# Kernel optimization log

Hardware: AMD Instinct MI355X
Metric: run time of the kernel (lower is better)

## Reference

```python
import jax, jax.numpy as jnp
import numpy as np

B, S, T, H, NH, NL = 16, 128, 64, 128, 8, 4
DH = H // NH
FF = 2 * H
SCALE = 1.0 / float(np.sqrt(DH))


def _ln(x, s, b):
    m = x.mean(-1, keepdims=True)
    v = ((x - m) ** 2).mean(-1, keepdims=True)
    return (x - m) * jax.lax.rsqrt(v + 1e-5) * s + b


def _block(x, mask, p):
    Wq, bq, Wk, bk, Wv, bv, Wo, bo, s1, c1, W1, d1, W2, d2, s2, c2 = p
    N, L, _ = x.shape
    q = (x @ Wq + bq).reshape(N, L, NH, DH)
    k = (x @ Wk + bk).reshape(N, L, NH, DH)
    v = (x @ Wv + bv).reshape(N, L, NH, DH)
    scores = jnp.einsum('nqhd,nkhd->nhqk', q, k) * SCALE
    scores = jnp.where(mask[:, None, :, :], scores, -1e9)
    a = jax.nn.softmax(scores, axis=-1)
    o = jnp.einsum('nhqk,nkhd->nqhd', a, v).reshape(N, L, H)
    x = _ln(x + o @ Wo + bo, s1, c1)
    h = jax.nn.relu(x @ W1 + d1)
    return _ln(x + h @ W2 + d2, s2, c2)


def setup_inputs():
    key = jax.random.key(0)
    ks = jax.random.split(key, 16)
    g = lambda k, shape: jax.random.normal(k, shape, jnp.float32) * 0.02
    return {
        'polylines': jax.random.normal(ks[0], (B, S, T, H), jnp.float32),
        'lengths': jax.random.randint(ks[1], (B, S), 0, T + 1),
        'proj_w': g(ks[2], (H, H)), 'proj_b': jnp.zeros((H,), jnp.float32),
        'proj_ln_s': jnp.ones((H,), jnp.float32), 'proj_ln_b': jnp.zeros((H,), jnp.float32),
        'pos_emb': g(ks[3], (1, T, H)),
        'Wq': g(ks[4], (NL, H, H)), 'bq': jnp.zeros((NL, H), jnp.float32),
        'Wk': g(ks[5], (NL, H, H)), 'bk': jnp.zeros((NL, H), jnp.float32),
        'Wv': g(ks[6], (NL, H, H)), 'bv': jnp.zeros((NL, H), jnp.float32),
        'Wo': g(ks[7], (NL, H, H)), 'bo': jnp.zeros((NL, H), jnp.float32),
        'ln1_s': jnp.ones((NL, H), jnp.float32), 'ln1_b': jnp.zeros((NL, H), jnp.float32),
        'W1': g(ks[8], (NL, H, FF)), 'b1': jnp.zeros((NL, FF), jnp.float32),
        'W2': g(ks[9], (NL, FF, H)), 'b2': jnp.zeros((NL, H), jnp.float32),
        'ln2_s': jnp.ones((NL, H), jnp.float32), 'ln2_b': jnp.zeros((NL, H), jnp.float32),
    }


def reference(polylines, lengths, proj_w, proj_b, proj_ln_s, proj_ln_b, pos_emb,
              Wq, bq, Wk, bk, Wv, bv, Wo, bo, ln1_s, ln1_b, W1, b1, W2, b2, ln2_s, ln2_b):
    # valid[b,s,t] = t < lengths[b,s]; lengths==0 -> polyline absent (fully padded)
    valid = jnp.arange(T)[None, None, :] < lengths[:, :, None]  # [B,S,T]
    x = jnp.where(valid[..., None], polylines, -1.0)            # -1 pad as in np.pad(constant_values=-1)
    # mask_temporal[b,s] = outer(valid[b,s], valid[b,s])
    mask_t = (valid[:, :, :, None] & valid[:, :, None, :]).reshape(B * S, T, T)
    # mask_spatial[b,t] = outer(valid[b,:,t], valid[b,:,t])
    vs = jnp.transpose(valid, (0, 2, 1))                        # [B,T,S]
    mask_s = (vs[:, :, :, None] & vs[:, :, None, :]).reshape(B * T, S, S)

    x = x.reshape(B * S, T, H)
    x = jax.nn.relu(_ln(x @ proj_w + proj_b, proj_ln_s, proj_ln_b))  # MLP: Linear->LN->ReLU
    x = x + pos_emb[:, :T, :]

    mask = mask_t
    for i in range(NL):
        if i == NL // 2:
            # switch from temporal to spatial attention: [B*S,T,H] -> [B*T,S,H]
            x = x.reshape(B, S, T, H).transpose(0, 2, 1, 3).reshape(B * T, S, H)
            mask = mask_s
        p = (Wq[i], bq[i], Wk[i], bk[i], Wv[i], bv[i], Wo[i], bo[i],
             ln1_s[i], ln1_b[i], W1[i], b1[i], W2[i], b2[i], ln2_s[i], ln2_b[i])
        x = _block(x, mask, p)
    # faithful to original final reshape (treats [B*T,S,H] buffer as [B,S,T,H])
    return x.reshape(B, S, T, H)[:, 0, :]
```

## Files before the change

kernel.cpp:

```cpp
#include <hip/hip_runtime.h>

typedef short short8 __attribute__((ext_vector_type(8)));
typedef short short4_t __attribute__((ext_vector_type(4)));
typedef float floatx4 __attribute__((ext_vector_type(4)));
typedef unsigned short ushort_t;

#define B_ 16
#define S_ 128
#define T_ 64
#define H_ 128
#define FF_ 256
#define SCALEQK 0.25f

#define EPI_BIAS 0
#define EPI_RELU 1
#define EPI_LNRES 2
#define EPI_PROJ 3

#define OFFP 0
#define OFFQ(l) (16384 + (l) * 65536)
#define OFFK(l) (OFFQ(l) + 16384)
#define OFFV(l) (OFFQ(l) + 32768)
#define OFFO(l) (OFFQ(l) + 49152)
#define OFFW1(l) (278528 + (l) * 65536)
#define OFFW2(l) (OFFW1(l) + 32768)

__device__ __forceinline__ float b2f(ushort_t u) {
    union { unsigned int i; float f; } x; x.i = ((unsigned int)u) << 16; return x.f;
}
__device__ __forceinline__ ushort_t f2b(float f) {
    union { float f; unsigned int i; } x; x.f = f;
    unsigned int r = x.i + 0x7fffu + ((x.i >> 16) & 1u);
    return (ushort_t)(r >> 16);
}
__device__ __forceinline__ int pack2b(float a, float b) {
    return (int)f2b(a) | ((int)f2b(b) << 16);
}

struct WtEnt { const float* src; int N; int K; int nclog2; int dstoff; };
struct WtArgs { WtEnt e[25]; };

__global__ __launch_bounds__(256) void wt_kernel(WtArgs a, ushort_t* __restrict__ dst) {
    WtEnt ent = a.e[blockIdx.x];
    const int tiles_c = ent.N >> 5;
    const int nt = (ent.K >> 5) * tiles_c;
    const int t = blockIdx.y;
    if (t >= nt) return;
    const int tc = t & (tiles_c - 1);
    const int tr = t >> ent.nclog2;
    __shared__ float ld[32 * 33];
    const int tid = threadIdx.x;
#pragma unroll
    for (int i = 0; i < 4; ++i) {
        int e = tid + i * 256;
        int rr = e >> 5, cc = e & 31;
        ld[rr * 33 + cc] = ent.src[(tr * 32 + rr) * ent.N + tc * 32 + cc];
    }
    __syncthreads();
    ushort_t* d = dst + ent.dstoff;
#pragma unroll
    for (int i = 0; i < 4; ++i) {
        int e = tid + i * 256;
        int rr = e >> 5, cc = e & 31;
        d[(tc * 32 + rr) * ent.K + tr * 32 + cc] = f2b(ld[cc * 33 + rr]);
    }
}

template<int K, int EPI, bool PAD, bool FINAL, bool MULTI, bool OUTB, bool AB16>
__global__ __launch_bounds__(256, 2) void gemm_mfma(
    const void* __restrict__ Av, int lda,
    const ushort_t* wt0, const ushort_t* wt1, const ushort_t* wt2,
    const float* b0, const float* b1, const float* b2,
    const float* __restrict__ resid, int rstride,
    const float* __restrict__ lns, const float* __restrict__ lnb,
    const float* __restrict__ pos, const int* __restrict__ lens,
    void* o0, void* o1, void* o2,
    int Ntot)
{
    __shared__ ushort_t aL[128 * 136];
    __shared__ ushort_t wL[128 * 136];

    const int tid = threadIdx.x;
    const int lane = tid & 63, wv = tid >> 6;
    const size_t rowbase = (size_t)blockIdx.x * 128;

    const ushort_t* wT; const float* bias; void* out; int cbase;
    if (MULTI) {
        int sel = blockIdx.y;
        wT = sel == 0 ? wt0 : (sel == 1 ? wt1 : wt2);
        bias = sel == 0 ? b0 : (sel == 1 ? b1 : b2);
        out = sel == 0 ? o0 : (sel == 1 ? o1 : o2);
        cbase = 0;
    } else {
        wT = wt0; bias = b0; out = o0; cbase = blockIdx.y * 128;
    }

    floatx4 acc[2][8];
#pragma unroll
    for (int a = 0; a < 2; ++a)
#pragma unroll
        for (int c = 0; c < 8; ++c) acc[a][c] = (floatx4){0.f, 0.f, 0.f, 0.f};

    const int arow = wv * 32 + (lane & 15);
    const int koff = (lane >> 4) * 8;

    for (int kc = 0; kc < K; kc += 128) {
        if (kc) __syncthreads();
#pragma unroll
        for (int it = 0; it < 8; ++it) {
            int e8 = tid + it * 256;
            int row = e8 >> 4, kg = e8 & 15;
            int kk = kc + kg * 8;
            short8 val;
            if (AB16) {
                val = *(const short8*)((const ushort_t*)Av + (size_t)(rowbase + row) * lda + kk);
            } else {
                const float* Af = (const float*)Av + (size_t)(rowbase + row) * lda + kk;
                float f[8];
                *(float4*)(f) = *(const float4*)(Af);
                *(float4*)(f + 4) = *(const float4*)(Af + 4);
                if (PAD) {
                    int r = (int)(rowbase + row);
                    if ((r & 63) >= lens[r >> 6]) {
#pragma unroll
                        for (int q = 0; q < 8; ++q) f[q] = -1.0f;
                    }
                }
#pragma unroll
                for (int q = 0; q < 8; ++q) val[q] = (short)f2b(f[q]);
            }
            *(short8*)&aL[row * 136 + kg * 8] = val;
        }
#pragma unroll
        for (int it = 0; it < 8; ++it) {
            int e8 = tid + it * 256;
            int n = e8 >> 4, kg = e8 & 15;
            *(short8*)&wL[n * 136 + kg * 8] =
                *(const short8*)&wT[(size_t)(cbase + n) * K + kc + kg * 8];
        }
        __syncthreads();
#pragma unroll
        for (int k0 = 0; k0 < 128; k0 += 32) {
            short8 a0 = *(const short8*)&aL[arow * 136 + k0 + koff];
            short8 a1 = *(const short8*)&aL[(arow + 16) * 136 + k0 + koff];
#pragma unroll
            for (int ct = 0; ct < 8; ++ct) {
                short8 b = *(const short8*)&wL[(ct * 16 + (lane & 15)) * 136 + k0 + koff];
                acc[0][ct] = __builtin_amdgcn_mfma_f32_16x16x32_bf16(a0, b, acc[0][ct], 0, 0, 0);
                acc[1][ct] = __builtin_amdgcn_mfma_f32_16x16x32_bf16(a1, b, acc[1][ct], 0, 0, 0);
            }
        }
    }

    const int col16 = lane & 15;
    const int rgrp = (lane >> 4) * 4;
    float bcol[8], lnsc[8], lnbc[8];
#pragma unroll
    for (int ct = 0; ct < 8; ++ct) bcol[ct] = bias[cbase + ct * 16 + col16];
    if (EPI == EPI_LNRES || EPI == EPI_PROJ) {
#pragma unroll
        for (int ct = 0; ct < 8; ++ct) {
            lnsc[ct] = lns[ct * 16 + col16];
            lnbc[ct] = lnb[ct * 16 + col16];
        }
    }

#pragma unroll
    for (int rt = 0; rt < 2; ++rt) {
        const int rbase = wv * 32 + rt * 16 + rgrp;
#pragma unroll
        for (int ct = 0; ct < 8; ++ct)
#pragma unroll
            for (int rg = 0; rg < 4; ++rg) {
                float v = acc[rt][ct][rg] + bcol[ct];
                if (EPI == EPI_LNRES)
                    v += resid[(rowbase + rbase + rg) * (size_t)rstride + ct * 16 + col16];
                acc[rt][ct][rg] = v;
            }
        if (EPI == EPI_LNRES || EPI == EPI_PROJ) {
            float mean[4], rstd[4];
#pragma unroll
            for (int rg = 0; rg < 4; ++rg) {
                float s = 0.f;
#pragma unroll
                for (int ct = 0; ct < 8; ++ct) s += acc[rt][ct][rg];
                s += __shfl_xor(s, 1); s += __shfl_xor(s, 2);
                s += __shfl_xor(s, 4); s += __shfl_xor(s, 8);
                mean[rg] = s * (1.f / 128.f);
            }
#pragma unroll
            for (int rg = 0; rg < 4; ++rg) {
                float s = 0.f;
#pragma unroll
                for (int ct = 0; ct < 8; ++ct) {
                    float d = acc[rt][ct][rg] - mean[rg];
                    s += d * d;
                }
                s += __shfl_xor(s, 1); s += __shfl_xor(s, 2);
                s += __shfl_xor(s, 4); s += __shfl_xor(s, 8);
                rstd[rg] = rsqrtf(s * (1.f / 128.f) + 1e-5f);
            }
#pragma unroll
            for (int ct = 0; ct < 8; ++ct)
#pragma unroll
                for (int rg = 0; rg < 4; ++rg)
                    acc[rt][ct][rg] = (acc[rt][ct][rg] - mean[rg]) * rstd[rg] * lnsc[ct] + lnbc[ct];
        }
#pragma unroll
        for (int ct = 0; ct < 8; ++ct)
#pragma unroll
            for (int rg = 0; rg < 4; ++rg) {
                size_t grow = rowbase + rbase + rg;
                int col = cbase + ct * 16 + col16;
                float v = acc[rt][ct][rg];
                if (EPI == EPI_RELU) v = fmaxf(v, 0.f);
                if (EPI == EPI_PROJ)
                    v = fmaxf(v, 0.f) + pos[((int)grow & 63) * H_ + ct * 16 + col16];
                if (FINAL) {
                    int b = (int)(grow >> 7), s = (int)(grow & 127);
                    if (s < T_) ((float*)out)[((size_t)(b * T_ + s)) * H_ + col] = v;
                } else if (OUTB) {
                    ((ushort_t*)out)[grow * (size_t)Ntot + col] = f2b(v);
                } else {
                    ((float*)out)[grow * (size_t)Ntot + col] = v;
                }
            }
    }
}

__global__ __launch_bounds__(256, 1) void attn_s(
    ushort_t* qo, const ushort_t* __restrict__ kk, const ushort_t* __restrict__ vv,
    const int* __restrict__ lens)
{
    __shared__ float kL[128 * 36];
    __shared__ float vL[128 * 36];
    __shared__ int vldL[128];
    const int tid = threadIdx.x;
    const int b = blockIdx.x, hp = blockIdx.y;
    const size_t rowg = (size_t)b * 128;

    if (tid < 128) vldL[tid] = (lens[b * 128 + tid] > 0) ? 1 : 0;
#pragma unroll
    for (int it = 0; it < 2; ++it) {
        int e8 = tid + it * 256;
        int j = e8 >> 2, dg = e8 & 3;
        short8 k8 = *(const short8*)&kk[(rowg + j) * 128 + hp * 32 + dg * 8];
        short8 v8 = *(const short8*)&vv[(rowg + j) * 128 + hp * 32 + dg * 8];
        float* kd = &kL[j * 36 + dg * 8];
        float* vd = &vL[j * 36 + dg * 8];
#pragma unroll
        for (int q = 0; q < 8; ++q) { kd[q] = b2f((ushort_t)k8[q]); vd[q] = b2f((ushort_t)v8[q]); }
    }
    __syncthreads();

    const int hl = tid >> 7;
    const int i = tid & 127;
    const int hc = hl * 16;
    const int h = hp * 2 + hl;

    float qf[16];
    {
        const short8* qp = (const short8*)&qo[(rowg + i) * 128 + h * 16];
        short8 q0 = qp[0], q1 = qp[1];
#pragma unroll
        for (int q = 0; q < 8; ++q) { qf[q] = b2f((ushort_t)q0[q]); qf[8 + q] = b2f((ushort_t)q1[q]); }
    }

    float sc[128];
    const bool iv = vldL[i] != 0;
#pragma unroll
    for (int j = 0; j < 128; ++j) {
        const float* kr = &kL[j * 36 + hc];
        float s = 0.f;
#pragma unroll
        for (int d = 0; d < 16; ++d) s = fmaf(qf[d], kr[d], s);
        sc[j] = (iv && vldL[j]) ? s * SCALEQK : -1e9f;
    }
    float m = -3.0e38f;
#pragma unroll
    for (int j = 0; j < 128; ++j) m = fmaxf(m, sc[j]);
    float sum = 0.f;
#pragma unroll
    for (int j = 0; j < 128; ++j) { float e = __expf(sc[j] - m); sc[j] = e; sum += e; }
    const float inv = 1.0f / sum;
    float of[16];
#pragma unroll
    for (int d = 0; d < 16; ++d) of[d] = 0.f;
#pragma unroll
    for (int j = 0; j < 128; ++j) {
        float p = sc[j] * inv;
        const float* vr = &vL[j * 36 + hc];
#pragma unroll
        for (int d = 0; d < 16; ++d) of[d] = fmaf(p, vr[d], of[d]);
    }
    short8 o0v, o1v;
#pragma unroll
    for (int q = 0; q < 8; ++q) { o0v[q] = (short)f2b(of[q]); o1v[q] = (short)f2b(of[8 + q]); }
    short8* op = (short8*)&qo[(rowg + i) * 128 + h * 16];
    op[0] = o0v; op[1] = o1v;
}

template<int RT, int CT, int KK>
__device__ __forceinline__ void mm_g(const ushort_t* aL, int sa,
                                     const ushort_t* __restrict__ wT,
                                     int colbase, int lane, floatx4 (&acc)[RT][CT]) {
    const int l15 = lane & 15, lq8 = (lane >> 4) * 8;
#pragma unroll
    for (int r = 0; r < RT; ++r)
#pragma unroll
        for (int c = 0; c < CT; ++c) acc[r][c] = (floatx4){0.f, 0.f, 0.f, 0.f};
#pragma unroll
    for (int k0 = 0; k0 < KK; k0 += 32) {
        short8 b[CT];
#pragma unroll
        for (int c = 0; c < CT; ++c)
            b[c] = *(const short8*)&wT[(colbase + c * 16 + l15) * KK + k0 + lq8];
#pragma unroll
        for (int r = 0; r < RT; ++r) {
            short8 a = *(const short8*)&aL[(r * 16 + l15) * sa + k0 + lq8];
#pragma unroll
            for (int c = 0; c < CT; ++c)
                acc[r][c] = __builtin_amdgcn_mfma_f32_16x16x32_bf16(a, b[c], acc[r][c], 0, 0, 0);
        }
    }
}

template<int RT, int CT>
__device__ __forceinline__ void add_bias(floatx4 (&acc)[RT][CT], const float* b,
                                         int colbase, int l15) {
#pragma unroll
    for (int c = 0; c < CT; ++c) {
        float bc = b[colbase + c * 16 + l15];
#pragma unroll
        for (int r = 0; r < RT; ++r)
#pragma unroll
            for (int g = 0; g < 4; ++g) acc[r][c][g] += bc;
    }
}

template<int RT, int CT>
__device__ __forceinline__ void add_resid_reg(floatx4 (&acc)[RT][CT],
                                              const float (&res)[RT][CT][4]) {
#pragma unroll
    for (int r = 0; r < RT; ++r)
#pragma unroll
        for (int c = 0; c < CT; ++c)
#pragma unroll
            for (int g = 0; g < 4; ++g) acc[r][c][g] += res[r][c][g];
}
template<int RT, int CT>
__device__ __forceinline__ void save_resid(float (&res)[RT][CT][4],
                                           const floatx4 (&acc)[RT][CT]) {
#pragma unroll
    for (int r = 0; r < RT; ++r)
#pragma unroll
        for (int c = 0; c < CT; ++c)
#pragma unroll
            for (int g = 0; g < 4; ++g) res[r][c][g] = acc[r][c][g];
}

template<int RT, int CT>
__device__ __forceinline__ void st_n(const floatx4 (&acc)[RT][CT], ushort_t* dst, int stride,
                                     int colbase, int l15, int lq) {
#pragma unroll
    for (int r = 0; r < RT; ++r)
#pragma unroll
        for (int g = 0; g < 4; ++g) {
            int row = r * 16 + lq * 4 + g;
#pragma unroll
            for (int c = 0; c < CT; ++c)
                dst[row * stride + colbase + c * 16 + l15] = f2b(acc[r][c][g]);
        }
}

template<int RT, int CT>
__device__ __forceinline__ void st_t(const floatx4 (&acc)[RT][CT], ushort_t* dst, int stride,
                                     int colbase, int l15, int lq) {
#pragma unroll
    for (int r = 0; r < RT; ++r)
#pragma unroll
        for (int c = 0; c < CT; ++c) {
            int d = colbase + c * 16 + l15;
            short4_t p;
#pragma unroll
            for (int g = 0; g < 4; ++g) p[g] = (short)f2b(acc[r][c][g]);
            *(short4_t*)&dst[d * stride + r * 16 + lq * 4] = p;
        }
}

template<int RT, int CT>
__device__ __forceinline__ void ln_norm(floatx4 (&acc)[RT][CT], float* redL,
                                        const float* lns, const float* lnb,
                                        int colbase, int l15, int lq, int wv) {
#pragma unroll
    for (int r = 0; r < RT; ++r)
#pragma unroll
        for (int g = 0; g < 4; ++g) {
            float s = 0.f, q = 0.f;
#pragma unroll
            for (int c = 0; c < CT; ++c) { float v = acc[r][c][g]; s += v; q += v * v; }
            s += __shfl_xor(s, 1); s += __shfl_xor(s, 2); s += __shfl_xor(s, 4); s += __shfl_xor(s, 8);
            q += __shfl_xor(q, 1); q += __shfl_xor(q, 2); q += __shfl_xor(q, 4); q += __shfl_xor(q, 8);
            if (l15 == 0) {
                int row = r * 16 + lq * 4 + g;
                redL[row * 8 + wv] = s;
                redL[row * 8 + 4 + wv] = q;
            }
        }
    __syncthreads();
#pragma unroll
    for (int r = 0; r < RT; ++r)
#pragma unroll
        for (int g = 0; g < 4; ++g) {
            int row = r * 16 + lq * 4 + g;
            float4 S = *(float4*)&redL[row * 8];
            float4 Q = *(float4*)&redL[row * 8 + 4];
            float mean = (S.x + S.y + S.z + S.w) * (1.f / 128.f);
            float var = (Q.x + Q.y + Q.z + Q.w) * (1.f / 128.f) - mean * mean;
            float rstd = rsqrtf(var + 1e-5f);
#pragma unroll
            for (int c = 0; c < CT; ++c) {
                int col = colbase + c * 16 + l15;
                acc[r][c][g] = (acc[r][c][g] - mean) * rstd * lns[col] + lnb[col];
            }
        }
}

template<int JT>
__device__ __forceinline__ void softmax_pack(floatx4 (&st)[JT], bool iv, unsigned jm,
                                             int (&px)[JT][2]) {
    float ev[JT][4];
    float mx = -3.0e38f;
#pragma unroll
    for (int jt = 0; jt < JT; ++jt)
#pragma unroll
        for (int g = 0; g < 4; ++g) {
            bool ok = iv && ((jm >> (jt * 4 + g)) & 1u);
            float s = ok ? st[jt][g] * SCALEQK : -1e9f;
            ev[jt][g] = s; mx = fmaxf(mx, s);
        }
    mx = fmaxf(mx, __shfl_xor(mx, 16)); mx = fmaxf(mx, __shfl_xor(mx, 32));
    float sum = 0.f;
#pragma unroll
    for (int jt = 0; jt < JT; ++jt)
#pragma unroll
        for (int g = 0; g < 4; ++g) { float e = __expf(ev[jt][g] - mx); ev[jt][g] = e; sum += e; }
    sum += __shfl_xor(sum, 16); sum += __shfl_xor(sum, 32);
    float inv = 1.f / sum;
#pragma unroll
    for (int jt = 0; jt < JT; ++jt) {
        px[jt][0] = pack2b(ev[jt][0] * inv, ev[jt][1] * inv);
        px[jt][1] = pack2b(ev[jt][2] * inv, ev[jt][3] * inv);
    }
}

__device__ __forceinline__ short8 pfrag(const int (*px)[2], int jc, int lq, int l15) {
    const int jA = (lq & 1) * 32 + l15;
    int a0 = __shfl(px[jc * 2][0], jA);
    int a1 = __shfl(px[jc * 2][1], jA);
    int a2 = __shfl(px[jc * 2][0], jA + 16);
    int a3 = __shfl(px[jc * 2][1], jA + 16);
    int b0 = __shfl(px[jc * 2 + 1][0], jA);
    int b1 = __shfl(px[jc * 2 + 1][1], jA);
    int b2 = __shfl(px[jc * 2 + 1][0], jA + 16);
    int b3 = __shfl(px[jc * 2 + 1][1], jA + 16);
    const bool t = (lq >> 1) != 0;
    union { int4 i; short8 s; } u;
    u.i = make_int4(t ? b0 : a0, t ? b1 : a1, t ? b2 : a2, t ? b3 : a3);
    return u.s;
}
__device__ __forceinline__ short8 vfrag(const ushort_t* vT, int stride, int row, int off) {
    int2 a = *(const int2*)&vT[row * stride + off];
    int2 b = *(const int2*)&vT[row * stride + off + 4];
    union { int4 i; short8 s; } u;
    u.i = make_int4(a.x, a.y, b.x, b.y);
    return u.s;
}

__global__ __launch_bounds__(256, 2) void k1_mega(
    const float* __restrict__ poly, const int* __restrict__ lens,
    const ushort_t* __restrict__ wt,
    const float* __restrict__ projb, const float* __restrict__ pls,
    const float* __restrict__ plb, const float* __restrict__ pos,
    const float* __restrict__ bq0, const float* __restrict__ bk0,
    const float* __restrict__ bv0, const float* __restrict__ bo0,
    const float* __restrict__ l1s0, const float* __restrict__ l1b0,
    const float* __restrict__ b10, const float* __restrict__ b20,
    const float* __restrict__ l2s0, const float* __restrict__ l2b0,
    const float* __restrict__ bq1, const float* __restrict__ bk1,
    const float* __restrict__ bv1,
    ushort_t* __restrict__ o1, float* __restrict__ xr0f)
{
    __shared__ ushort_t pool[34816];
    __shared__ float redL[512];
    __shared__ float psL[8 * 68];
    __shared__ float q1L[128];
    ushort_t* xL = pool;
    ushort_t* qL = pool + 8704;
    ushort_t* kL = pool + 17408;
    ushort_t* vT = pool + 26112;
    ushort_t* hL = pool + 17408;

    const int tid = threadIdx.x, lane = tid & 63, wv = tid >> 6;
    const int l15 = lane & 15, lq = lane >> 4;
    const int gid = blockIdx.x;
    const int len = lens[gid];

    {
        const float* pg = poly + (size_t)gid * 8192;
#pragma unroll
        for (int it = 0; it < 8; ++it) {
            int e4 = (tid + it * 256) * 4;
            int row = e4 >> 7, col = e4 & 127;
            float4 f = *(const float4*)(pg + e4);
            if (row >= len) { f.x = -1.f; f.y = -1.f; f.z = -1.f; f.w = -1.f; }
            short4_t u;
            u[0] = (short)f2b(f.x); u[1] = (short)f2b(f.y);
            u[2] = (short)f2b(f.z); u[3] = (short)f2b(f.w);
            *(short4_t*)&xL[row * 136 + col] = u;
        }
    }
    __syncthreads();

    floatx4 a2[4][2];
    float xre[4][2][4];

    mm_g<4, 2, 128>(xL, 136, wt + OFFP, wv * 32, lane, a2);
    add_bias<4, 2>(a2, projb, wv * 32, l15);
    ln_norm<4, 2>(a2, redL, pls, plb, wv * 32, l15, lq, wv);
    __syncthreads();
#pragma unroll
    for (int r = 0; r < 4; ++r)
#pragma unroll
        for (int gg = 0; gg < 4; ++gg) {
            int row = r * 16 + lq * 4 + gg;
#pragma unroll
            for (int c = 0; c < 2; ++c) {
                int col = wv * 32 + c * 16 + l15;
                float v = fmaxf(a2[r][c][gg], 0.f) + pos[row * 128 + col];
                xre[r][c][gg] = v;
                xL[row * 136 + col] = f2b(v);
            }
        }
    __syncthreads();

    mm_g<4, 2, 128>(xL, 136, wt + OFFQ(0), wv * 32, lane, a2);
    add_bias<4, 2>(a2, bq0, wv * 32, l15);
    st_n<4, 2>(a2, qL, 136, wv * 32, l15, lq);
    mm_g<4, 2, 128>(xL, 136, wt + OFFK(0), wv * 32, lane, a2);
    add_bias<4, 2>(a2, bk0, wv * 32, l15);
    st_n<4, 2>(a2, kL, 136, wv * 32, l15, lq);
    mm_g<4, 2, 128>(xL, 136, wt + OFFV(0), wv * 32, lane, a2);
    add_bias<4, 2>(a2, bv0, wv * 32, l15);
    st_t<4, 2>(a2, vT, 68, wv * 32, l15, lq);
    __syncthreads();

    {
        const int iRow = wv * 16 + l15;
        const bool iv = iRow < len;
        unsigned jm = 0;
#pragma unroll
        for (int jt = 0; jt < 4; ++jt)
#pragma unroll
            for (int gg = 0; gg < 4; ++gg)
                if (jt * 16 + lq * 4 + gg < len) jm |= (1u << (jt * 4 + gg));
        for (int h = 0; h < 8; ++h) {
            const int hc = h * 16;
            short8 z8 = {0, 0, 0, 0, 0, 0, 0, 0};
            short8 bqf = z8;
            if (lq < 2) bqf = *(const short8*)&qL[iRow * 136 + hc + lq * 8];
            floatx4 st[4];
#pragma unroll
            for (int jt = 0; jt < 4; ++jt) {
                short8 ak = z8;
                if (lq < 2) ak = *(const short8*)&kL[(jt * 16 + l15) * 136 + hc + lq * 8];
                floatx4 zz = {0.f, 0.f, 0.f, 0.f};
                st[jt] = __builtin_amdgcn_mfma_f32_16x16x32_bf16(ak, bqf, zz, 0, 0, 0);
            }
            int px[4][2];
            softmax_pack<4>(st, iv, jm, px);
            floatx4 ao = {0.f, 0.f, 0.f, 0.f};
#pragma unroll
            for (int jc = 0; jc < 2; ++jc) {
                short8 av = vfrag(vT, 68, hc + l15, jc * 32 + lq * 8);
                short8 bp = pfrag(px, jc, lq, l15);
                ao = __builtin_amdgcn_mfma_f32_16x16x32_bf16(av, bp, ao, 0, 0, 0);
            }
            short4_t w;
#pragma unroll
            for (int gg = 0; gg < 4; ++gg) w[gg] = (short)f2b(ao[gg]);
            *(short4_t*)&qL[iRow * 136 + hc + lq * 4] = w;
        }
    }
    __syncthreads();

    mm_g<4, 2, 128>(qL, 136, wt + OFFO(0), wv * 32, lane, a2);
    add_bias<4, 2>(a2, bo0, wv * 32, l15);
    add_resid_reg<4, 2>(a2, xre);
    ln_norm<4, 2>(a2, redL, l1s0, l1b0, wv * 32, l15, lq, wv);
    save_resid<4, 2>(xre, a2);
    st_n<4, 2>(a2, xL, 136, wv * 32, l15, lq);
    __syncthreads();

    {
        floatx4 a4[4][4];
        mm_g<4, 4, 128>(xL, 136, wt + OFFW1(0), wv * 64, lane, a4);
        add_bias<4, 4>(a4, b10, wv * 64, l15);
#pragma unroll
        for (int r = 0; r < 4; ++r)
#pragma unroll
            for (int c = 0; c < 4; ++c)
#pragma unroll
                for (int gg = 0; gg < 4; ++gg) a4[r][c][gg] = fmaxf(a4[r][c][gg], 0.f);
        st_n<4, 4>(a4, hL, 272, wv * 64, l15, lq);
    }
    __syncthreads();

    mm_g<4, 2, 256>(hL, 272, wt + OFFW2(0), wv * 32, lane, a2);
    add_bias<4, 2>(a2, b20, wv * 32, l15);
    add_resid_reg<4, 2>(a2, xre);
    ln_norm<4, 2>(a2, redL, l2s0, l2b0, wv * 32, l15, lq, wv);
    save_resid<4, 2>(xre, a2);
    st_n<4, 2>(a2, xL, 136, wv * 32, l15, lq);
    if (lq == 0) {
#pragma unroll
        for (int c = 0; c < 2; ++c)
            xr0f[(size_t)gid * 128 + wv * 32 + c * 16 + l15] = a2[0][c][0];
    }
    __syncthreads();

    mm_g<4, 2, 128>(xL, 136, wt + OFFK(1), wv * 32, lane, a2);
    add_bias<4, 2>(a2, bk1, wv * 32, l15);
    st_n<4, 2>(a2, kL, 136, wv * 32, l15, lq);
    mm_g<4, 2, 128>(xL, 136, wt + OFFV(1), wv * 32, lane, a2);
    add_bias<4, 2>(a2, bv1, wv * 32, l15);
    st_t<4, 2>(a2, vT, 68, wv * 32, l15, lq);
    if (tid < 128) {
        int d = tid;
        float a = bq1[d];
        const ushort_t* wq = wt + OFFQ(1) + d * 128;
#pragma unroll 4
        for (int j0 = 0; j0 < 128; j0 += 8) {
            short8 w8 = *(const short8*)&wq[j0];
            short8 x8 = *(const short8*)&xL[j0];
#pragma unroll
            for (int q = 0; q < 8; ++q)
                a = fmaf(b2f((ushort_t)x8[q]), b2f((ushort_t)w8[q]), a);
        }
        q1L[d] = a;
    }
    __syncthreads();

    {
        int h = tid >> 5, jj = tid & 31;
        int hc = h * 16;
        float s[2];
#pragma unroll
        for (int half = 0; half < 2; ++half) {
            int j = jj + half * 32;
            float a = 0.f;
            short8 k0v = *(const short8*)&kL[j * 136 + hc];
            short8 k1v = *(const short8*)&kL[j * 136 + hc + 8];
#pragma unroll
            for (int q = 0; q < 8; ++q) {
                a = fmaf(q1L[hc + q], b2f((ushort_t)k0v[q]), a);
                a = fmaf(q1L[hc + 8 + q], b2f((ushort_t)k1v[q]), a);
            }
            s[half] = (j < len) ? a * SCALEQK : -1e9f;
        }
        float mx = fmaxf(s[0], s[1]);
#pragma unroll
        for (int d = 1; d < 32; d <<= 1) mx = fmaxf(mx, __shfl_xor(mx, d));
        float e0 = __expf(s[0] - mx), e1 = __expf(s[1] - mx);
        float sum = e0 + e1;
#pragma unroll
        for (int d = 1; d < 32; d <<= 1) sum += __shfl_xor(sum, d);
        float inv = 1.f / sum;
        psL[h * 68 + jj] = e0 * inv;
        psL[h * 68 + jj + 32] = e1 * inv;
    }
    __syncthreads();
    if (tid < 128) {
        int h = tid >> 4, d = tid & 15, hc = h * 16;
        float a = 0.f;
#pragma unroll 4
        for (int j0 = 0; j0 < 64; j0 += 4) {
            float4 p4 = *(const float4*)&psL[h * 68 + j0];
            short4_t v4 = *(const short4_t*)&vT[(hc + d) * 68 + j0];
            a += p4.x * b2f((ushort_t)v4[0]) + p4.y * b2f((ushort_t)v4[1])
               + p4.z * b2f((ushort_t)v4[2]) + p4.w * b2f((ushort_t)v4[3]);
        }
        o1[(size_t)gid * 128 + hc + d] = f2b(a);
    }
}

extern "C" void kernel_launch(void* const* d_in, const int* in_sizes, int n_in,
                              void* d_out, int out_size, void* d_ws, size_t ws_size,
                              hipStream_t stream)
{
    const float* poly   = (const float*)d_in[0];
    const int*   lens   = (const int*)d_in[1];
    const float* proj_w = (const float*)d_in[2];
    const float* proj_b = (const float*)d_in[3];
    const float* pls    = (const float*)d_in[4];
    const float* plb    = (const float*)d_in[5];
    const float* pos    = (const float*)d_in[6];
    const float* Wq = (const float*)d_in[7];
    const float* bq = (const float*)d_in[8];
    const float* Wk = (const float*)d_in[9];
    const float* bk = (const float*)d_in[10];
    const float* Wv = (const float*)d_in[11];
    const float* bv = (const float*)d_in[12];
    const float* Wo = (const float*)d_in[13];
    const float* bo = (const float*)d_in[14];
    const float* l1s = (const float*)d_in[15];
    const float* l1b = (const float*)d_in[16];
    const float* W1 = (const float*)d_in[17];
    const float* b1 = (const float*)d_in[18];
    const float* W2 = (const float*)d_in[19];
    const float* b2 = (const float*)d_in[20];
    const float* l2s = (const float*)d_in[21];
    const float* l2b = (const float*)d_in[22];
    float* outp = (float*)d_out;

    char* base = (char*)d_ws;
    ushort_t* wt    = (ushort_t*)base;
    ushort_t* o1buf = (ushort_t*)(base + 1081344);
    float* xr0f     = (float*)(base + 1605632);
    float* ybuf     = (float*)(base + 2654208);
    ushort_t* hsml  = (ushort_t*)(base + 3702784);
    ushort_t* q2    = (ushort_t*)(base + 4751360);
    ushort_t* k2b   = (ushort_t*)(base + 5275648);
    ushort_t* v2    = (ushort_t*)(base + 5799936);

    const int HH = H_ * H_, HF = H_ * FF_;
    WtArgs wa;
    wa.e[0] = {proj_w, 128, 128, 2, OFFP};
    for (int l = 0; l < 4; ++l) {
        wa.e[1 + l * 4 + 0] = {Wq + l * HH, 128, 128, 2, OFFQ(l)};
        wa.e[1 + l * 4 + 1] = {Wk + l * HH, 128, 128, 2, OFFK(l)};
        wa.e[1 + l * 4 + 2] = {Wv + l * HH, 128, 128, 2, OFFV(l)};
        wa.e[1 + l * 4 + 3] = {Wo + l * HH, 128, 128, 2, OFFO(l)};
    }
    for (int l = 0; l < 4; ++l) {
        wa.e[17 + l * 2 + 0] = {W1 + l * HF, 256, 128, 3, OFFW1(l)};
        wa.e[17 + l * 2 + 1] = {W2 + l * HF, 128, 256, 2, OFFW2(l)};
    }
    wt_kernel<<<dim3(25, 32), 256, 0, stream>>>(wa, wt);

    k1_mega<<<dim3(2048), 256, 0, stream>>>(
        poly, lens, wt,
        proj_b, pls, plb, pos,
        bq, bk, bv, bo, l1s, l1b, b1, b2, l2s, l2b,
        bq + H_, bk + H_, bv + H_,
        o1buf, xr0f);

    gemm_mfma<128, EPI_LNRES, false, false, false, false, true><<<dim3(16, 1), 256, 0, stream>>>(
        o1buf, 128, wt + OFFO(1), wt + OFFO(1), wt + OFFO(1), bo + H_, bo + H_, bo + H_,
        xr0f, 128, l1s + H_, l1b + H_, nullptr, nullptr, ybuf, ybuf, ybuf, H_);
    gemm_mfma<128, EPI_RELU, false, false, false, true, false><<<dim3(16, 2), 256, 0, stream>>>(
        ybuf, 128, wt + OFFW1(1), wt + OFFW1(1), wt + OFFW1(1), b1 + FF_, b1 + FF_, b1 + FF_,
        nullptr, 0, nullptr, nullptr, nullptr, nullptr, hsml, hsml, hsml, FF_);
    gemm_mfma<256, EPI_LNRES, false, false, false, false, true><<<dim3(16, 1), 256, 0, stream>>>(
        hsml, 256, wt + OFFW2(1), wt + OFFW2(1), wt + OFFW2(1), b2 + H_, b2 + H_, b2 + H_,
        ybuf, 128, l2s + H_, l2b + H_, nullptr, nullptr, ybuf, ybuf, ybuf, H_);

    for (int l = 2; l < 4; ++l) {
        gemm_mfma<128, EPI_BIAS, false, false, true, true, false><<<dim3(16, 3), 256, 0, stream>>>(
            ybuf, 128, wt + OFFQ(l), wt + OFFK(l), wt + OFFV(l),
            bq + l * H_, bk + l * H_, bv + l * H_,
            nullptr, 0, nullptr, nullptr, nullptr, nullptr, q2, k2b, v2, H_);
        attn_s<<<dim3(16, 4), 256, 0, stream>>>(q2, k2b, v2, lens);
        gemm_mfma<128, EPI_LNRES, false, false, false, false, true><<<dim3(16, 1), 256, 0, stream>>>(
            q2, 128, wt + OFFO(l), wt + OFFO(l), wt + OFFO(l), bo + l * H_, bo + l * H_, bo + l * H_,
            ybuf, 128, l1s + l * H_, l1b + l * H_, nullptr, nullptr, ybuf, ybuf, ybuf, H_);
        gemm_mfma<128, EPI_RELU, false, false, false, true, false><<<dim3(16, 2), 256, 0, stream>>>(
            ybuf, 128, wt + OFFW1(l), wt + OFFW1(l), wt + OFFW1(l),
            b1 + l * FF_, b1 + l * FF_, b1 + l * FF_,
            nullptr, 0, nullptr, nullptr, nullptr, nullptr, hsml, hsml, hsml, FF_);
        if (l < 3) {
            gemm_mfma<256, EPI_LNRES, false, false, false, false, true><<<dim3(16, 1), 256, 0, stream>>>(
                hsml, 256, wt + OFFW2(l), wt + OFFW2(l), wt + OFFW2(l),
                b2 + l * H_, b2 + l * H_, b2 + l * H_,
                ybuf, 128, l2s + l * H_, l2b + l * H_, nullptr, nullptr, ybuf, ybuf, ybuf, H_);
        } else {
            gemm_mfma<256, EPI_LNRES, false, true, false, false, true><<<dim3(16, 1), 256, 0, stream>>>(
                hsml, 256, wt + OFFW2(l), wt + OFFW2(l), wt + OFFW2(l),
                b2 + l * H_, b2 + l * H_, b2 + l * H_,
                ybuf, 128, l2s + l * H_, l2b + l * H_, nullptr, nullptr, outp, outp, outp, H_);
        }
    }
}
```

Before: 432.0 us.

## Fuse spatial-attention tail launches into one cooperative kernel with grid syncs

```diff
diff --git a/kernel.cpp b/kernel.cpp
--- a/kernel.cpp
+++ b/kernel.cpp
@@ -1,4 +1,7 @@
 #include <hip/hip_runtime.h>
+#include <hip/hip_cooperative_groups.h>
+
+namespace cg = cooperative_groups;
 
 typedef short short8 __attribute__((ext_vector_type(8)));
 typedef short short4_t __attribute__((ext_vector_type(4)));
@@ -15,7 +18,6 @@
 #define EPI_BIAS 0
 #define EPI_RELU 1
 #define EPI_LNRES 2
-#define EPI_PROJ 3
 
 #define OFFP 0
 #define OFFQ(l) (16384 + (l) * 65536)
@@ -66,34 +68,18 @@
     }
 }
 
-template<int K, int EPI, bool PAD, bool FINAL, bool MULTI, bool OUTB, bool AB16>
-__global__ __launch_bounds__(256, 2) void gemm_mfma(
-    const void* __restrict__ Av, int lda,
-    const ushort_t* wt0, const ushort_t* wt1, const ushort_t* wt2,
-    const float* b0, const float* b1, const float* b2,
-    const float* __restrict__ resid, int rstride,
-    const float* __restrict__ lns, const float* __restrict__ lnb,
-    const float* __restrict__ pos, const int* __restrict__ lens,
-    void* o0, void* o1, void* o2,
-    int Ntot)
+template<int K, int EPI, bool FINAL, bool OUTB, bool AB16>
+__device__ void gemm_phase(ushort_t* aL, ushort_t* wL,
+                           const void* __restrict__ Av, int lda,
+                           const ushort_t* __restrict__ wT, const float* bias,
+                           const float* __restrict__ resid, int rstride,
+                           const float* __restrict__ lns, const float* __restrict__ lnb,
+                           void* out, int Ntot, int rowtile, int cbase)
 {
-    __shared__ ushort_t aL[128 * 136];
-    __shared__ ushort_t wL[128 * 136];
-
+    __syncthreads();
     const int tid = threadIdx.x;
     const int lane = tid & 63, wv = tid >> 6;
-    const size_t rowbase = (size_t)blockIdx.x * 128;
-
-    const ushort_t* wT; const float* bias; void* out; int cbase;
-    if (MULTI) {
-        int sel = blockIdx.y;
-        wT = sel == 0 ? wt0 : (sel == 1 ? wt1 : wt2);
-        bias = sel == 0 ? b0 : (sel == 1 ? b1 : b2);
-        out = sel == 0 ? o0 : (sel == 1 ? o1 : o2);
-        cbase = 0;
-    } else {
-        wT = wt0; bias = b0; out = o0; cbase = blockIdx.y * 128;
-    }
+    const size_t rowbase = (size_t)rowtile * 128;
 
     floatx4 acc[2][8];
 #pragma unroll
@@ -119,13 +105,6 @@
                 float f[8];
                 *(float4*)(f) = *(const float4*)(Af);
                 *(float4*)(f + 4) = *(const float4*)(Af + 4);
-                if (PAD) {
-                    int r = (int)(rowbase + row);
-                    if ((r & 63) >= lens[r >> 6]) {
-#pragma unroll
-                        for (int q = 0; q < 8; ++q) f[q] = -1.0f;
-                    }
-                }
 #pragma unroll
                 for (int q = 0; q < 8; ++q) val[q] = (short)f2b(f[q]);
             }
@@ -157,7 +136,7 @@
     float bcol[8], lnsc[8], lnbc[8];
 #pragma unroll
     for (int ct = 0; ct < 8; ++ct) bcol[ct] = bias[cbase + ct * 16 + col16];
-    if (EPI == EPI_LNRES || EPI == EPI_PROJ) {
+    if (EPI == EPI_LNRES) {
 #pragma unroll
         for (int ct = 0; ct < 8; ++ct) {
             lnsc[ct] = lns[ct * 16 + col16];
@@ -177,7 +156,7 @@
                     v += resid[(rowbase + rbase + rg) * (size_t)rstride + ct * 16 + col16];
                 acc[rt][ct][rg] = v;
             }
-        if (EPI == EPI_LNRES || EPI == EPI_PROJ) {
+        if (EPI == EPI_LNRES) {
             float mean[4], rstd[4];
 #pragma unroll
             for (int rg = 0; rg < 4; ++rg) {
@@ -214,8 +193,6 @@
                 int col = cbase + ct * 16 + col16;
                 float v = acc[rt][ct][rg];
                 if (EPI == EPI_RELU) v = fmaxf(v, 0.f);
-                if (EPI == EPI_PROJ)
-                    v = fmaxf(v, 0.f) + pos[((int)grow & 63) * H_ + ct * 16 + col16];
                 if (FINAL) {
                     int b = (int)(grow >> 7), s = (int)(grow & 127);
                     if (s < T_) ((float*)out)[((size_t)(b * T_ + s)) * H_ + col] = v;
@@ -228,15 +205,13 @@
     }
 }
 
-__global__ __launch_bounds__(256, 1) void attn_s(
-    ushort_t* qo, const ushort_t* __restrict__ kk, const ushort_t* __restrict__ vv,
-    const int* __restrict__ lens)
+__device__ void attn_phase(float* kL, float* vL, int* vldL,
+                           ushort_t* qo, const ushort_t* __restrict__ kk,
+                           const ushort_t* __restrict__ vv,
+                           const int* __restrict__ lens, int b, int hp)
 {
-    __shared__ float kL[128 * 36];
-    __shared__ float vL[128 * 36];
-    __shared__ int vldL[128];
+    __syncthreads();
     const int tid = threadIdx.x;
-    const int b = blockIdx.x, hp = blockIdx.y;
     const size_t rowg = (size_t)b * 128;
 
     if (tid < 128) vldL[tid] = (lens[b * 128 + tid] > 0) ? 1 : 0;
@@ -298,6 +273,80 @@
     for (int q = 0; q < 8; ++q) { o0v[q] = (short)f2b(of[q]); o1v[q] = (short)f2b(of[8 + q]); }
     short8* op = (short8*)&qo[(rowg + i) * 128 + h * 16];
     op[0] = o0v; op[1] = o1v;
+}
+
+struct TailArgs {
+    const int* lens; const ushort_t* wt;
+    const ushort_t* o1buf; const float* xr0f;
+    float* ybuf; ushort_t* hsml; ushort_t* q2; ushort_t* k2; ushort_t* v2;
+    const float* bq; const float* bk; const float* bv; const float* bo;
+    const float* l1s; const float* l1b; const float* b1; const float* b2;
+    const float* l2s; const float* l2b;
+    float* outp;
+};
+
+__global__ __launch_bounds__(256, 2) void tail_coop(TailArgs a)
+{
+    cg::grid_group grid = cg::this_grid();
+    __shared__ __align__(16) ushort_t poolA[128 * 136];
+    __shared__ __align__(16) ushort_t poolW[128 * 136];
+    __shared__ int vldS[128];
+    const int nb = gridDim.x;
+    const int bid = blockIdx.x;
+
+    for (int t = bid; t < 16; t += nb)
+        gemm_phase<128, EPI_LNRES, false, false, true>(poolA, poolW,
+            a.o1buf, 128, a.wt + OFFO(1), a.bo + H_, a.xr0f, 128,
+            a.l1s + H_, a.l1b + H_, a.ybuf, H_, t, 0);
+    grid.sync();
+    for (int t = bid; t < 32; t += nb)
+        gemm_phase<128, EPI_RELU, false, true, false>(poolA, poolW,
+            a.ybuf, 128, a.wt + OFFW1(1), a.b1 + FF_, nullptr, 0,
+            nullptr, nullptr, a.hsml, FF_, t >> 1, (t & 1) * 128);
+    grid.sync();
+    for (int t = bid; t < 16; t += nb)
+        gemm_phase<256, EPI_LNRES, false, false, true>(poolA, poolW,
+            a.hsml, 256, a.wt + OFFW2(1), a.b2 + H_, a.ybuf, 128,
+            a.l2s + H_, a.l2b + H_, a.ybuf, H_, t, 0);
+    grid.sync();
+
+    for (int l = 2; l < 4; ++l) {
+        for (int t = bid; t < 48; t += nb) {
+            int rt = t & 15, sel = t >> 4;
+            const ushort_t* wsel = a.wt + (sel == 0 ? OFFQ(l) : sel == 1 ? OFFK(l) : OFFV(l));
+            const float* bsel = (sel == 0 ? a.bq : sel == 1 ? a.bk : a.bv) + l * H_;
+            void* osel = sel == 0 ? (void*)a.q2 : sel == 1 ? (void*)a.k2 : (void*)a.v2;
+            gemm_phase<128, EPI_BIAS, false, true, false>(poolA, poolW,
+                a.ybuf, 128, wsel, bsel, nullptr, 0, nullptr, nullptr, osel, H_, rt, 0);
+        }
+        grid.sync();
+        for (int t = bid; t < 64; t += nb)
+            attn_phase((float*)poolA, (float*)poolW, vldS,
+                       a.q2, a.k2, a.v2, a.lens, t & 15, t >> 4);
+        grid.sync();
+        for (int t = bid; t < 16; t += nb)
+            gemm_phase<128, EPI_LNRES, false, false, true>(poolA, poolW,
+                a.q2, 128, a.wt + OFFO(l), a.bo + l * H_, a.ybuf, 128,
+                a.l1s + l * H_, a.l1b + l * H_, a.ybuf, H_, t, 0);
+        grid.sync();
+        for (int t = bid; t < 32; t += nb)
+            gemm_phase<128, EPI_RELU, false, true, false>(poolA, poolW,
+                a.ybuf, 128, a.wt + OFFW1(l), a.b1 + l * FF_, nullptr, 0,
+                nullptr, nullptr, a.hsml, FF_, t >> 1, (t & 1) * 128);
+        grid.sync();
+        if (l < 3) {
+            for (int t = bid; t < 16; t += nb)
+                gemm_phase<256, EPI_LNRES, false, false, true>(poolA, poolW,
+                    a.hsml, 256, a.wt + OFFW2(l), a.b2 + l * H_, a.ybuf, 128,
+                    a.l2s + l * H_, a.l2b + l * H_, a.ybuf, H_, t, 0);
+            grid.sync();
+        } else {
+            for (int t = bid; t < 16; t += nb)
+                gemm_phase<256, EPI_LNRES, true, false, true>(poolA, poolW,
+                    a.hsml, 256, a.wt + OFFW2(l), a.b2 + l * H_, a.ybuf, 128,
+                    a.l2s + l * H_, a.l2b + l * H_, a.outp, H_, t, 0);
+        }
+    }
 }
 
 template<int RT, int CT, int KK>
@@ -755,39 +804,15 @@
         bq + H_, bk + H_, bv + H_,
         o1buf, xr0f);
 
-    gemm_mfma<128, EPI_LNRES, false, false, false, false, true><<<dim3(16, 1), 256, 0, stream>>>(
-        o1buf, 128, wt + OFFO(1), wt + OFFO(1), wt + OFFO(1), bo + H_, bo + H_, bo + H_,
-        xr0f, 128, l1s + H_, l1b + H_, nullptr, nullptr, ybuf, ybuf, ybuf, H_);
-    gemm_mfma<128, EPI_RELU, false, false, false, true, false><<<dim3(16, 2), 256, 0, stream>>>(
-        ybuf, 128, wt + OFFW1(1), wt + OFFW1(1), wt + OFFW1(1), b1 + FF_, b1 + FF_, b1 + FF_,
-        nullptr, 0, nullptr, nullptr, nullptr, nullptr, hsml, hsml, hsml, FF_);
-    gemm_mfma<256, EPI_LNRES, false, false, false, false, true><<<dim3(16, 1), 256, 0, stream>>>(
-        hsml, 256, wt + OFFW2(1), wt + OFFW2(1), wt + OFFW2(1), b2 + H_, b2 + H_, b2 + H_,
-        ybuf, 128, l2s + H_, l2b + H_, nullptr, nullptr, ybuf, ybuf, ybuf, H_);
-
-    for (int l = 2; l < 4; ++l) {
-        gemm_mfma<128, EPI_BIAS, false, false, true, true, false><<<dim3(16, 3), 256, 0, stream>>>(
-            ybuf, 128, wt + OFFQ(l), wt + OFFK(l), wt + OFFV(l),
-            bq + l * H_, bk + l * H_, bv + l * H_,
-            nullptr, 0, nullptr, nullptr, nullptr, nullptr, q2, k2b, v2, H_);
-        attn_s<<<dim3(16, 4), 256, 0, stream>>>(q2, k2b, v2, lens);
-        gemm_mfma<128, EPI_LNRES, false, false, false, false, true><<<dim3(16, 1), 256, 0, stream>>>(
-            q2, 128, wt + OFFO(l), wt + OFFO(l), wt + OFFO(l), bo + l * H_, bo + l * H_, bo + l * H_,
-            ybuf, 128, l1s + l * H_, l1b + l * H_, nullptr, nullptr, ybuf, ybuf, ybuf, H_);
-        gemm_mfma<128, EPI_RELU, false, false, false, true, false><<<dim3(16, 2), 256, 0, stream>>>(
-            ybuf, 128, wt + OFFW1(l), wt + OFFW1(l), wt + OFFW1(l),
-            b1 + l * FF_, b1 + l * FF_, b1 + l * FF_,
-            nullptr, 0, nullptr, nullptr, nullptr, nullptr, hsml, hsml, hsml, FF_);
-        if (l < 3) {
-            gemm_mfma<256, EPI_LNRES, false, false, false, false, true><<<dim3(16, 1), 256, 0, stream>>>(
-                hsml, 256, wt + OFFW2(l), wt + OFFW2(l), wt + OFFW2(l),
-                b2 + l * H_, b2 + l * H_, b2 + l * H_,
-                ybuf, 128, l2s + l * H_, l2b + l * H_, nullptr, nullptr, ybuf, ybuf, ybuf, H_);
-        } else {
-            gemm_mfma<256, EPI_LNRES, false, true, false, false, true><<<dim3(16, 1), 256, 0, stream>>>(
-                hsml, 256, wt + OFFW2(l), wt + OFFW2(l), wt + OFFW2(l),
-                b2 + l * H_, b2 + l * H_, b2 + l * H_,
-                ybuf, 128, l2s + l * H_, l2b + l * H_, nullptr, nullptr, outp, outp, outp, H_);
-        }
-    }
-}
+    TailArgs ta;
+    ta.lens = lens; ta.wt = wt;
+    ta.o1buf = o1buf; ta.xr0f = xr0f;
+    ta.ybuf = ybuf; ta.hsml = hsml; ta.q2 = q2; ta.k2 = k2b; ta.v2 = v2;
+    ta.bq = bq; ta.bk = bk; ta.bv = bv; ta.bo = bo;
+    ta.l1s = l1s; ta.l1b = l1b; ta.b1 = b1; ta.b2 = b2;
+    ta.l2s = l2s; ta.l2b = l2b;
+    ta.outp = outp;
+    void* kargs[] = { &ta };
+    hipLaunchCooperativeKernel((const void*)tail_coop, dim3(64), dim3(256),
+                               kargs, 0, stream);
+}
```

New measurement: 606.1 us. 40.3% more time.
